# Performance work log

Hardware: AMD Instinct MI355X
Metric: run time of the kernel (lower is better)

Reference implementation:

```python
import jax, jax.numpy as jnp
import numpy as np

N_NODES = 100000
N_EDGES = 3200000
F_IN = 128
HIDDEN = 16
F_OUT = 2


def setup_inputs() -> dict:
    key = jax.random.key(0)
    k1, k2, k3, k4 = jax.random.split(key, 4)
    x = jax.random.normal(k1, (N_NODES, F_IN), dtype=jnp.float32)
    edge_index = jax.random.randint(k2, (2, N_EDGES), 0, N_NODES, dtype=jnp.int64)
    # Glorot-ish init like torch_geometric's GCNConv linear layers
    W1 = jax.random.normal(k3, (F_IN, HIDDEN), dtype=jnp.float32) * (1.0 / np.sqrt(F_IN))
    b1 = jnp.zeros((HIDDEN,), dtype=jnp.float32)
    W2 = jax.random.normal(k4, (HIDDEN, F_OUT), dtype=jnp.float32) * (1.0 / np.sqrt(HIDDEN))
    b2 = jnp.zeros((F_OUT,), dtype=jnp.float32)
    return {"x": x, "edge_index": edge_index, "W1": W1, "b1": b1, "W2": W2, "b2": b2}


def _gcn_conv(x, src, dst, W, b, num_nodes):
    """PyG GCNConv: out = D^{-1/2}(A+I)D^{-1/2} X W + b (self-loops included in src/dst)."""
    h = x @ W  # [N, F_out]
    ones = jnp.ones(src.shape[0], dtype=h.dtype)
    deg = jax.ops.segment_sum(ones, dst, num_segments=num_nodes)  # in-degree incl. self-loop
    deg_inv_sqrt = jnp.where(deg > 0, jax.lax.rsqrt(jnp.maximum(deg, 1.0)), 0.0)
    norm = deg_inv_sqrt[src] * deg_inv_sqrt[dst]  # [E+N]
    msg = h[src] * norm[:, None]  # gather + scale: [E+N, F_out]
    out = jax.ops.segment_sum(msg, dst, num_segments=num_nodes)  # scatter-add
    return out + b


def reference(x, edge_index, W1, b1, W2, b2):
    num_nodes = x.shape[0]
    self_loops = jnp.arange(num_nodes, dtype=edge_index.dtype)
    src = jnp.concatenate([edge_index[0], self_loops])
    dst = jnp.concatenate([edge_index[1], self_loops])
    h = jax.nn.relu(_gcn_conv(x, src, dst, W1, b1, num_nodes))
    # F.dropout(training=self.training) is identity in eval mode
    out = _gcn_conv(h, src, dst, W2, b2, num_nodes)
    return out
```

## Files before the change

### kernel.cpp

```cpp
#include <hip/hip_runtime.h>

#define N_NODES 100000
#define N_EDGES 3200000
#define F_IN    128
#define HIDDEN  16
#define F_OUT   2

#define BSZ     128
#define NB      782
#define NPAD    (NB * BSZ)
#define G       512
#define EPB     (N_EDGES / G)
#define DUMMY_E 100000u

typedef float  f32x4 __attribute__((ext_vector_type(4)));
typedef float  f32x2 __attribute__((ext_vector_type(2)));
typedef _Float16 half8 __attribute__((ext_vector_type(8)));
typedef _Float16 half4 __attribute__((ext_vector_type(4)));

__global__ __launch_bounds__(256) void k_hist(const int* __restrict__ dst,
                                              unsigned* __restrict__ blockHist) {
    __shared__ unsigned hist[NB];
    int t = threadIdx.x, g = blockIdx.x;
    for (int i = t; i < NB; i += 256) hist[i] = 0u;
    __syncthreads();
    int base = g * EPB;
    for (int i = t; i < EPB; i += 256) atomicAdd(&hist[dst[base + i] >> 7], 1u);
    __syncthreads();
    for (int i = t; i < NB; i += 256) blockHist[i * G + g] = hist[i];
}

__global__ __launch_bounds__(G) void k_scan_blocks(unsigned* __restrict__ blockHist,
                                                   unsigned* __restrict__ total) {
    __shared__ unsigned s[G];
    int b = blockIdx.x, t = threadIdx.x;
    unsigned v = blockHist[b * G + t];
    s[t] = v;
    __syncthreads();
    for (int off = 1; off < G; off <<= 1) {
        unsigned xv = (t >= off) ? s[t - off] : 0u;
        __syncthreads();
        s[t] += xv;
        __syncthreads();
    }
    blockHist[b * G + t] = s[t] - v;
    if (t == G - 1) total[b] = s[t];
}

__global__ __launch_bounds__(1024) void k_scan_buckets(const unsigned* __restrict__ total,
                                                       unsigned* __restrict__ bucketBase,
                                                       int* __restrict__ rowstart) {
    __shared__ unsigned s[1024];
    int t = threadIdx.x;
    unsigned v = (t < NB) ? total[t] : 0u;
    s[t] = v;
    __syncthreads();
    for (int off = 1; off < 1024; off <<= 1) {
        unsigned xv = (t >= off) ? s[t - off] : 0u;
        __syncthreads();
        s[t] += xv;
        __syncthreads();
    }
    if (t < NB) bucketBase[t] = s[t] - v;
    if (t == 1023) {
        bucketBase[NB] = s[t];
        rowstart[N_NODES] = (int)s[t];
    }
}

__global__ __launch_bounds__(256) void k_scatter(const int* __restrict__ src,
                                                 const int* __restrict__ dst,
                                                 const unsigned* __restrict__ blockHist,
                                                 const unsigned* __restrict__ bucketBase,
                                                 unsigned* __restrict__ adj) {
    __shared__ unsigned stage[EPB];
    __shared__ unsigned short stage_b[EPB];
    __shared__ unsigned hist[NB];
    __shared__ unsigned lstart[NB];
    __shared__ unsigned gbase[NB];
    __shared__ unsigned ssum[256];
    int t = threadIdx.x, g = blockIdx.x;
    for (int i = t; i < NB; i += 256) {
        hist[i] = 0u;
        gbase[i] = bucketBase[i] + blockHist[i * G + g];
    }
    __syncthreads();
    int base = g * EPB;
    const int* srcg = src + base;
    const int* dstg = dst + base;
    for (int i = t; i < EPB; i += 256) atomicAdd(&hist[(unsigned)dstg[i] >> 7], 1u);
    __syncthreads();
    int i0 = t * 4;
    unsigned v0 = (i0 + 0 < NB) ? hist[i0 + 0] : 0u;
    unsigned v1 = (i0 + 1 < NB) ? hist[i0 + 1] : 0u;
    unsigned v2 = (i0 + 2 < NB) ? hist[i0 + 2] : 0u;
    unsigned v3 = (i0 + 3 < NB) ? hist[i0 + 3] : 0u;
    unsigned my = v0 + v1 + v2 + v3;
    ssum[t] = my;
    __syncthreads();
    for (int off = 1; off < 256; off <<= 1) {
        unsigned xv = (t >= off) ? ssum[t - off] : 0u;
        __syncthreads();
        ssum[t] += xv;
        __syncthreads();
    }
    unsigned e0 = ssum[t] - my;
    __syncthreads();
    unsigned e1 = e0 + v0, e2 = e1 + v1, e3 = e2 + v2;
    if (i0 + 0 < NB) { lstart[i0 + 0] = e0; hist[i0 + 0] = e0; }
    if (i0 + 1 < NB) { lstart[i0 + 1] = e1; hist[i0 + 1] = e1; }
    if (i0 + 2 < NB) { lstart[i0 + 2] = e2; hist[i0 + 2] = e2; }
    if (i0 + 3 < NB) { lstart[i0 + 3] = e3; hist[i0 + 3] = e3; }
    __syncthreads();
    for (int i = t; i < EPB; i += 256) {
        int s = srcg[i], d = dstg[i];
        unsigned bkt = (unsigned)d >> 7;
        unsigned pos = atomicAdd(&hist[bkt], 1u);
        stage[pos] = ((unsigned)(d & 127) << 17) | (unsigned)s;
        stage_b[pos] = (unsigned short)bkt;
    }
    __syncthreads();
    for (int j = t; j < EPB; j += 256) {
        unsigned bkt = stage_b[j];
        adj[gbase[bkt] + (j - lstart[bkt])] = stage[j];
    }
}

__global__ __launch_bounds__(256) void k_sortbucket(const unsigned* __restrict__ adj,
                                                    const unsigned* __restrict__ bucketBase,
                                                    unsigned* __restrict__ adj2,
                                                    int* __restrict__ rowstart,
                                                    float* __restrict__ dinv) {
    __shared__ unsigned hist[BSZ];
    __shared__ unsigned sc[BSZ];
    __shared__ unsigned cur[BSZ];
    int b = blockIdx.x, t = threadIdx.x;
    if (t < BSZ) hist[t] = 0u;
    __syncthreads();
    int e0 = (int)bucketBase[b], e1 = (int)bucketBase[b + 1];
    for (int i = e0 + t; i < e1; i += 256) atomicAdd(&hist[adj[i] >> 17], 1u);
    __syncthreads();
    if (t < BSZ) sc[t] = hist[t];
    __syncthreads();
    for (int off = 1; off < BSZ; off <<= 1) {
        unsigned a = 0;
        if (t < BSZ && t >= off) a = sc[t - off];
        __syncthreads();
        if (t < BSZ) sc[t] += a;
        __syncthreads();
    }
    if (t < BSZ) {
        unsigned excl = sc[t] - hist[t];
        cur[t] = (unsigned)e0 + excl;
        int node = b * BSZ + t;
        if (node < N_NODES) {
            rowstart[node] = e0 + (int)excl;
            dinv[node] = rsqrtf((float)(hist[t] + 1u));
        }
    }
    __syncthreads();
    for (int i = e0 + t; i < e1; i += 256) {
        unsigned v = adj[i];
        unsigned pos = atomicAdd(&cur[v >> 17], 1u);
        adj2[pos] = v & 0x1FFFFu;
    }
}

#define MM1_NODES 64
#define SXP 132
__global__ __launch_bounds__(256) void k_mm1(const float* __restrict__ x,
                                             const float* __restrict__ W1,
                                             const float* __restrict__ dinv,
                                             half4* __restrict__ hs) {
    __shared__ float sW[F_IN * HIDDEN];
    __shared__ float sX[MM1_NODES * SXP];
    int t = threadIdx.x;
    for (int i = t; i < F_IN * HIDDEN; i += 256) sW[i] = W1[i];
    int node0 = blockIdx.x * MM1_NODES;
    const float4* xv = (const float4*)(x + (size_t)node0 * F_IN);
    int maxv = (N_NODES - node0) * (F_IN / 4);
    if (maxv < 0) maxv = 0;
    for (int i = t; i < MM1_NODES * (F_IN / 4); i += 256) {
        if (i < maxv) {
            int nl = i >> 5, f4 = i & 31;
            ((float4*)(sX + nl * SXP))[f4] = xv[i];
        }
    }
    __syncthreads();
    int lane4 = t & 3;
    int nl = t >> 2;
    int n = node0 + nl;
    if (n >= NPAD) return;
    if (n >= N_NODES) {
        half4 hz = {(_Float16)0.f, (_Float16)0.f, (_Float16)0.f, (_Float16)0.f};
        hs[(size_t)n * 4 + lane4] = hz;
        return;
    }
    const float4* sWv = (const float4*)sW;
    float4 a = {0.f, 0.f, 0.f, 0.f};
    #pragma unroll 8
    for (int f = 0; f < F_IN; ++f) {
        float xval = sX[nl * SXP + f];
        float4 w = sWv[f * 4 + lane4];
        a.x = fmaf(xval, w.x, a.x);
        a.y = fmaf(xval, w.y, a.y);
        a.z = fmaf(xval, w.z, a.z);
        a.w = fmaf(xval, w.w, a.w);
    }
    float dv = dinv[n];
    half4 h; h[0] = (_Float16)(a.x * dv); h[1] = (_Float16)(a.y * dv);
    h[2] = (_Float16)(a.z * dv); h[3] = (_Float16)(a.w * dv);
    hs[(size_t)n * 4 + lane4] = h;
}

__global__ __launch_bounds__(256) void k_agg1(const unsigned* __restrict__ adj2,
                                              const int* __restrict__ rowstart,
                                              const char* __restrict__ hs,
                                              const float* __restrict__ dinv,
                                              float* __restrict__ out1) {
    int g = blockIdx.x * 256 + threadIdx.x;
    int node = g >> 1, le = g & 1;
    if (node >= N_NODES) return;
    int rs = rowstart[node], re = rowstart[node + 1];
    unsigned le16 = (unsigned)le * 16u;
    unsigned dummy_off = DUMMY_E * 32u + le16;

    float a0 = 0.f, a1 = 0.f, a2 = 0.f, a3 = 0.f, a4 = 0.f, a5 = 0.f, a6 = 0.f, a7 = 0.f;
    f32x4 w0, w1, w2, w3, w4, w5, w6, w7;

#define GL1(dst, o) asm volatile("global_load_dwordx4 %0, %1, %2" \
    : "=v"(dst) : "v"(o), "s"(hs) : "memory");
#define AC1(w_) { half8 h8; __builtin_memcpy(&h8, &w_, 16); \
    a0 += (float)h8[0]; a1 += (float)h8[1]; a2 += (float)h8[2]; a3 += (float)h8[3]; \
    a4 += (float)h8[4]; a5 += (float)h8[5]; a6 += (float)h8[6]; a7 += (float)h8[7]; }

    for (int bs = rs; bs < re; bs += 8) {
        const unsigned* ap = adj2 + bs;
        unsigned j0 = ap[0], j1 = ap[1], j2 = ap[2], j3 = ap[3];
        unsigned j4 = ap[4], j5 = ap[5], j6 = ap[6], j7 = ap[7];
        unsigned o0 = (bs + 0 < re) ? (j0 << 5) + le16 : dummy_off;
        unsigned o1 = (bs + 1 < re) ? (j1 << 5) + le16 : dummy_off;
        unsigned o2 = (bs + 2 < re) ? (j2 << 5) + le16 : dummy_off;
        unsigned o3 = (bs + 3 < re) ? (j3 << 5) + le16 : dummy_off;
        unsigned o4 = (bs + 4 < re) ? (j4 << 5) + le16 : dummy_off;
        unsigned o5 = (bs + 5 < re) ? (j5 << 5) + le16 : dummy_off;
        unsigned o6 = (bs + 6 < re) ? (j6 << 5) + le16 : dummy_off;
        unsigned o7 = (bs + 7 < re) ? (j7 << 5) + le16 : dummy_off;
        GL1(w0, o0) GL1(w1, o1) GL1(w2, o2) GL1(w3, o3)
        GL1(w4, o4) GL1(w5, o5) GL1(w6, o6) GL1(w7, o7)
        asm volatile("s_waitcnt vmcnt(0)" ::: "memory");
        __builtin_amdgcn_sched_barrier(0);
        AC1(w0) AC1(w1) AC1(w2) AC1(w3) AC1(w4) AC1(w5) AC1(w6) AC1(w7)
    }
    const _Float16* selfrow = (const _Float16*)(hs + (size_t)node * 32 + le16);
    float dv = dinv[node];
    float4 q0, q1;
    q0.x = dv * (a0 + (float)selfrow[0]); q0.y = dv * (a1 + (float)selfrow[1]);
    q0.z = dv * (a2 + (float)selfrow[2]); q0.w = dv * (a3 + (float)selfrow[3]);
    q1.x = dv * (a4 + (float)selfrow[4]); q1.y = dv * (a5 + (float)selfrow[5]);
    q1.z = dv * (a6 + (float)selfrow[6]); q1.w = dv * (a7 + (float)selfrow[7]);
    float* op = out1 + (size_t)node * HIDDEN + le * 8;
    *(float4*)(op + 0) = q0;
    *(float4*)(op + 4) = q1;
}

__global__ __launch_bounds__(256) void k_mm2(const float* __restrict__ out1,
                                             const float* __restrict__ b1,
                                             const float* __restrict__ W2,
                                             const float* __restrict__ dinv,
                                             float2* __restrict__ hs2) {
    int n = blockIdx.x * 256 + threadIdx.x;
    if (n >= NPAD) return;
    if (n >= N_NODES) {
        float2 z = {0.f, 0.f};
        hs2[n] = z;
        return;
    }
    float a0 = 0.f, a1 = 0.f;
    #pragma unroll
    for (int kk = 0; kk < HIDDEN; ++kk) {
        float v = fmaxf(out1[(size_t)n * HIDDEN + kk] + b1[kk], 0.f);
        a0 = fmaf(v, W2[kk * F_OUT + 0], a0);
        a1 = fmaf(v, W2[kk * F_OUT + 1], a1);
    }
    float dv = dinv[n];
    float2 h2; h2.x = a0 * dv; h2.y = a1 * dv;
    hs2[n] = h2;
}

__global__ __launch_bounds__(256) void k_agg2(const unsigned* __restrict__ adj2,
                                              const int* __restrict__ rowstart,
                                              const char* __restrict__ hs2,
                                              const float* __restrict__ dinv,
                                              const float* __restrict__ b2,
                                              float2* __restrict__ out) {
    int node = blockIdx.x * 256 + threadIdx.x;
    if (node >= N_NODES) return;
    int rs = rowstart[node], re = rowstart[node + 1];
    unsigned dummy_off = DUMMY_E * 8u;

    float a0 = 0.f, a1 = 0.f;
    f32x2 w0, w1, w2, w3, w4, w5, w6, w7;

#define GL2(dst, o) asm volatile("global_load_dwordx2 %0, %1, %2" \
    : "=v"(dst) : "v"(o), "s"(hs2) : "memory");

    for (int bs = rs; bs < re; bs += 8) {
        const unsigned* ap = adj2 + bs;
        unsigned j0 = ap[0], j1 = ap[1], j2 = ap[2], j3 = ap[3];
        unsigned j4 = ap[4], j5 = ap[5], j6 = ap[6], j7 = ap[7];
        unsigned o0 = (bs + 0 < re) ? (j0 << 3) : dummy_off;
        unsigned o1 = (bs + 1 < re) ? (j1 << 3) : dummy_off;
        unsigned o2 = (bs + 2 < re) ? (j2 << 3) : dummy_off;
        unsigned o3 = (bs + 3 < re) ? (j3 << 3) : dummy_off;
        unsigned o4 = (bs + 4 < re) ? (j4 << 3) : dummy_off;
        unsigned o5 = (bs + 5 < re) ? (j5 << 3) : dummy_off;
        unsigned o6 = (bs + 6 < re) ? (j6 << 3) : dummy_off;
        unsigned o7 = (bs + 7 < re) ? (j7 << 3) : dummy_off;
        GL2(w0, o0) GL2(w1, o1) GL2(w2, o2) GL2(w3, o3)
        GL2(w4, o4) GL2(w5, o5) GL2(w6, o6) GL2(w7, o7)
        asm volatile("s_waitcnt vmcnt(0)" ::: "memory");
        __builtin_amdgcn_sched_barrier(0);
        a0 += w0[0] + w1[0] + w2[0] + w3[0] + w4[0] + w5[0] + w6[0] + w7[0];
        a1 += w0[1] + w1[1] + w2[1] + w3[1] + w4[1] + w5[1] + w6[1] + w7[1];
    }
    const float2* h2p = (const float2*)hs2;
    float2 selfv = h2p[node];
    float dv = dinv[node];
    float2 r;
    r.x = fmaf(dv, a0 + selfv.x, b2[0]);
    r.y = fmaf(dv, a1 + selfv.y, b2[1]);
    out[node] = r;
}

extern "C" void kernel_launch(void* const* d_in, const int* in_sizes, int n_in,
                              void* d_out, int out_size, void* d_ws, size_t ws_size,
                              hipStream_t stream) {
    const float* x   = (const float*)d_in[0];
    const int*   ei  = (const int*)d_in[1];
    const int*   srcv = ei;
    const int*   dstv = ei + N_EDGES;
    const float* W1  = (const float*)d_in[2];
    const float* b1  = (const float*)d_in[3];
    const float* W2  = (const float*)d_in[4];
    const float* b2  = (const float*)d_in[5];
    float* out = (float*)d_out;

    char* w = (char*)d_ws;
    unsigned* adj        = (unsigned*)w;  w += (size_t)N_EDGES * 4;
    float*    out1       = (float*)adj;
    unsigned* adj2       = (unsigned*)w;  w += (size_t)(N_EDGES + 8) * 4;
    unsigned* blockHist  = (unsigned*)w;  w += (size_t)NB * G * 4;
    unsigned* total      = (unsigned*)w;  w += (size_t)NB * 4;
    unsigned* bucketBase = (unsigned*)w;  w += (size_t)(NB + 1) * 4;
    int*      rowstart   = (int*)w;       w += (size_t)(N_NODES + 1) * 4;
    w = (char*)(((size_t)w + 15) & ~(size_t)15);
    float* dinv  = (float*)w;  w += (size_t)N_NODES * 4;
    char*  hs    = w;          w += (size_t)NPAD * HIDDEN * 2;
    float* hs2   = (float*)w;

    k_hist        <<<G, 256, 0, stream>>>(dstv, blockHist);
    k_scan_blocks <<<NB, G, 0, stream>>>(blockHist, total);
    k_scan_buckets<<<1, 1024, 0, stream>>>(total, bucketBase, rowstart);
    k_scatter     <<<G, 256, 0, stream>>>(srcv, dstv, blockHist, bucketBase, adj);
    k_sortbucket  <<<NB, 256, 0, stream>>>(adj, bucketBase, adj2, rowstart, dinv);
    k_mm1         <<<NPAD / MM1_NODES, 256, 0, stream>>>(x, W1, dinv, (half4*)hs);
    k_agg1        <<<(2 * NPAD) / 256, 256, 0, stream>>>(adj2, rowstart, hs, dinv, out1);
    k_mm2         <<<(NPAD + 255) / 256, 256, 0, stream>>>(out1, b1, W2, dinv, (float2*)hs2);
    k_agg2        <<<(NPAD + 255) / 256, 256, 0, stream>>>(adj2, rowstart, (const char*)hs2,
                                                           dinv, b2, (float2*)out);
}
```

Measured before the change: 138.3 us.

## Fuse second-layer transform into agg1, widen buckets, and split shared histograms

Folds the bias, ReLU and W2 projection into the first aggregation kernel, using a lane-pair shuffle to reduce the two halves. This removes the k_mm2 launch and the round trip of the 16-wide intermediate through global memory. The bucket size doubles to 256 nodes, so the bucket count halves, and the scan kernels and sort blocks are resized to match. Histogram kernels now read int2 and alternate threads between two shared histograms to reduce atomic contention. The catch is that each bucket sort block has more work and uses larger shared buffers.

```diff
diff --git a/kernel.cpp b/kernel.cpp
--- a/kernel.cpp
+++ b/kernel.cpp
@@ -6,8 +6,8 @@
 #define HIDDEN  16
 #define F_OUT   2
 
-#define BSZ     128
-#define NB      782
+#define BSZ     256
+#define NB      391
 #define NPAD    (NB * BSZ)
 #define G       512
 #define EPB     (N_EDGES / G)
@@ -20,14 +20,20 @@
 
 __global__ __launch_bounds__(256) void k_hist(const int* __restrict__ dst,
                                               unsigned* __restrict__ blockHist) {
-    __shared__ unsigned hist[NB];
+    __shared__ unsigned h0[NB];
+    __shared__ unsigned h1[NB];
     int t = threadIdx.x, g = blockIdx.x;
-    for (int i = t; i < NB; i += 256) hist[i] = 0u;
-    __syncthreads();
-    int base = g * EPB;
-    for (int i = t; i < EPB; i += 256) atomicAdd(&hist[dst[base + i] >> 7], 1u);
-    __syncthreads();
-    for (int i = t; i < NB; i += 256) blockHist[i * G + g] = hist[i];
+    for (int i = t; i < NB; i += 256) { h0[i] = 0u; h1[i] = 0u; }
+    __syncthreads();
+    const int2* d2 = (const int2*)(dst + g * EPB);
+    unsigned* myh = (t & 1) ? h1 : h0;
+    for (int i = t; i < EPB / 2; i += 256) {
+        int2 v = d2[i];
+        atomicAdd(&myh[(unsigned)v.x >> 8], 1u);
+        atomicAdd(&myh[(unsigned)v.y >> 8], 1u);
+    }
+    __syncthreads();
+    for (int i = t; i < NB; i += 256) blockHist[i * G + g] = h0[i] + h1[i];
 }
 
 __global__ __launch_bounds__(G) void k_scan_blocks(unsigned* __restrict__ blockHist,
@@ -47,22 +53,22 @@
     if (t == G - 1) total[b] = s[t];
 }
 
-__global__ __launch_bounds__(1024) void k_scan_buckets(const unsigned* __restrict__ total,
-                                                       unsigned* __restrict__ bucketBase,
-                                                       int* __restrict__ rowstart) {
-    __shared__ unsigned s[1024];
+__global__ __launch_bounds__(512) void k_scan_buckets(const unsigned* __restrict__ total,
+                                                      unsigned* __restrict__ bucketBase,
+                                                      int* __restrict__ rowstart) {
+    __shared__ unsigned s[512];
     int t = threadIdx.x;
     unsigned v = (t < NB) ? total[t] : 0u;
     s[t] = v;
     __syncthreads();
-    for (int off = 1; off < 1024; off <<= 1) {
+    for (int off = 1; off < 512; off <<= 1) {
         unsigned xv = (t >= off) ? s[t - off] : 0u;
         __syncthreads();
         s[t] += xv;
         __syncthreads();
     }
     if (t < NB) bucketBase[t] = s[t] - v;
-    if (t == 1023) {
+    if (t == 511) {
         bucketBase[NB] = s[t];
         rowstart[N_NODES] = (int)s[t];
     }
@@ -76,26 +82,29 @@
     __shared__ unsigned stage[EPB];
     __shared__ unsigned short stage_b[EPB];
     __shared__ unsigned hist[NB];
+    __shared__ unsigned h1[NB];
     __shared__ unsigned lstart[NB];
     __shared__ unsigned gbase[NB];
     __shared__ unsigned ssum[256];
     int t = threadIdx.x, g = blockIdx.x;
     for (int i = t; i < NB; i += 256) {
-        hist[i] = 0u;
+        hist[i] = 0u; h1[i] = 0u;
         gbase[i] = bucketBase[i] + blockHist[i * G + g];
     }
     __syncthreads();
-    int base = g * EPB;
-    const int* srcg = src + base;
-    const int* dstg = dst + base;
-    for (int i = t; i < EPB; i += 256) atomicAdd(&hist[(unsigned)dstg[i] >> 7], 1u);
-    __syncthreads();
-    int i0 = t * 4;
-    unsigned v0 = (i0 + 0 < NB) ? hist[i0 + 0] : 0u;
-    unsigned v1 = (i0 + 1 < NB) ? hist[i0 + 1] : 0u;
-    unsigned v2 = (i0 + 2 < NB) ? hist[i0 + 2] : 0u;
-    unsigned v3 = (i0 + 3 < NB) ? hist[i0 + 3] : 0u;
-    unsigned my = v0 + v1 + v2 + v3;
+    const int2* s2 = (const int2*)(src + g * EPB);
+    const int2* d2 = (const int2*)(dst + g * EPB);
+    unsigned* myh = (t & 1) ? h1 : hist;
+    for (int i = t; i < EPB / 2; i += 256) {
+        int2 v = d2[i];
+        atomicAdd(&myh[(unsigned)v.x >> 8], 1u);
+        atomicAdd(&myh[(unsigned)v.y >> 8], 1u);
+    }
+    __syncthreads();
+    int i0 = t * 2;
+    unsigned v0 = (i0 + 0 < NB) ? hist[i0 + 0] + h1[i0 + 0] : 0u;
+    unsigned v1 = (i0 + 1 < NB) ? hist[i0 + 1] + h1[i0 + 1] : 0u;
+    unsigned my = v0 + v1;
     ssum[t] = my;
     __syncthreads();
     for (int off = 1; off < 256; off <<= 1) {
@@ -106,18 +115,20 @@
     }
     unsigned e0 = ssum[t] - my;
     __syncthreads();
-    unsigned e1 = e0 + v0, e2 = e1 + v1, e3 = e2 + v2;
+    unsigned e1 = e0 + v0;
     if (i0 + 0 < NB) { lstart[i0 + 0] = e0; hist[i0 + 0] = e0; }
     if (i0 + 1 < NB) { lstart[i0 + 1] = e1; hist[i0 + 1] = e1; }
-    if (i0 + 2 < NB) { lstart[i0 + 2] = e2; hist[i0 + 2] = e2; }
-    if (i0 + 3 < NB) { lstart[i0 + 3] = e3; hist[i0 + 3] = e3; }
-    __syncthreads();
-    for (int i = t; i < EPB; i += 256) {
-        int s = srcg[i], d = dstg[i];
-        unsigned bkt = (unsigned)d >> 7;
-        unsigned pos = atomicAdd(&hist[bkt], 1u);
-        stage[pos] = ((unsigned)(d & 127) << 17) | (unsigned)s;
-        stage_b[pos] = (unsigned short)bkt;
+    __syncthreads();
+    for (int i = t; i < EPB / 2; i += 256) {
+        int2 sv = s2[i], dv = d2[i];
+        unsigned bkt0 = (unsigned)dv.x >> 8;
+        unsigned pos0 = atomicAdd(&hist[bkt0], 1u);
+        stage[pos0] = ((unsigned)(dv.x & 255) << 17) | (unsigned)sv.x;
+        stage_b[pos0] = (unsigned short)bkt0;
+        unsigned bkt1 = (unsigned)dv.y >> 8;
+        unsigned pos1 = atomicAdd(&hist[bkt1], 1u);
+        stage[pos1] = ((unsigned)(dv.y & 255) << 17) | (unsigned)sv.y;
+        stage_b[pos1] = (unsigned short)bkt1;
     }
     __syncthreads();
     for (int j = t; j < EPB; j += 256) {
@@ -135,28 +146,25 @@
     __shared__ unsigned sc[BSZ];
     __shared__ unsigned cur[BSZ];
     int b = blockIdx.x, t = threadIdx.x;
-    if (t < BSZ) hist[t] = 0u;
+    hist[t] = 0u;
     __syncthreads();
     int e0 = (int)bucketBase[b], e1 = (int)bucketBase[b + 1];
     for (int i = e0 + t; i < e1; i += 256) atomicAdd(&hist[adj[i] >> 17], 1u);
     __syncthreads();
-    if (t < BSZ) sc[t] = hist[t];
+    sc[t] = hist[t];
     __syncthreads();
     for (int off = 1; off < BSZ; off <<= 1) {
-        unsigned a = 0;
-        if (t < BSZ && t >= off) a = sc[t - off];
-        __syncthreads();
-        if (t < BSZ) sc[t] += a;
-        __syncthreads();
-    }
-    if (t < BSZ) {
-        unsigned excl = sc[t] - hist[t];
-        cur[t] = (unsigned)e0 + excl;
-        int node = b * BSZ + t;
-        if (node < N_NODES) {
-            rowstart[node] = e0 + (int)excl;
-            dinv[node] = rsqrtf((float)(hist[t] + 1u));
-        }
+        unsigned a = (t >= off) ? sc[t - off] : 0u;
+        __syncthreads();
+        sc[t] += a;
+        __syncthreads();
+    }
+    unsigned excl = sc[t] - hist[t];
+    cur[t] = (unsigned)e0 + excl;
+    int node = b * BSZ + t;
+    if (node < N_NODES) {
+        rowstart[node] = e0 + (int)excl;
+        dinv[node] = rsqrtf((float)(hist[t] + 1u));
     }
     __syncthreads();
     for (int i = e0 + t; i < e1; i += 256) {
@@ -217,10 +225,15 @@
                                               const int* __restrict__ rowstart,
                                               const char* __restrict__ hs,
                                               const float* __restrict__ dinv,
-                                              float* __restrict__ out1) {
+                                              const float* __restrict__ b1,
+                                              const float* __restrict__ W2,
+                                              float2* __restrict__ hs2) {
     int g = blockIdx.x * 256 + threadIdx.x;
     int node = g >> 1, le = g & 1;
-    if (node >= N_NODES) return;
+    if (node >= N_NODES) {
+        if (le == 0 && node < NPAD) { float2 z = {0.f, 0.f}; hs2[node] = z; }
+        return;
+    }
     int rs = rowstart[node], re = rowstart[node + 1];
     unsigned le16 = (unsigned)le * 16u;
     unsigned dummy_off = DUMMY_E * 32u + le16;
@@ -254,38 +267,29 @@
     }
     const _Float16* selfrow = (const _Float16*)(hs + (size_t)node * 32 + le16);
     float dv = dinv[node];
-    float4 q0, q1;
-    q0.x = dv * (a0 + (float)selfrow[0]); q0.y = dv * (a1 + (float)selfrow[1]);
-    q0.z = dv * (a2 + (float)selfrow[2]); q0.w = dv * (a3 + (float)selfrow[3]);
-    q1.x = dv * (a4 + (float)selfrow[4]); q1.y = dv * (a5 + (float)selfrow[5]);
-    q1.z = dv * (a6 + (float)selfrow[6]); q1.w = dv * (a7 + (float)selfrow[7]);
-    float* op = out1 + (size_t)node * HIDDEN + le * 8;
-    *(float4*)(op + 0) = q0;
-    *(float4*)(op + 4) = q1;
-}
-
-__global__ __launch_bounds__(256) void k_mm2(const float* __restrict__ out1,
-                                             const float* __restrict__ b1,
-                                             const float* __restrict__ W2,
-                                             const float* __restrict__ dinv,
-                                             float2* __restrict__ hs2) {
-    int n = blockIdx.x * 256 + threadIdx.x;
-    if (n >= NPAD) return;
-    if (n >= N_NODES) {
-        float2 z = {0.f, 0.f};
-        hs2[n] = z;
-        return;
-    }
-    float a0 = 0.f, a1 = 0.f;
-    #pragma unroll
-    for (int kk = 0; kk < HIDDEN; ++kk) {
-        float v = fmaxf(out1[(size_t)n * HIDDEN + kk] + b1[kk], 0.f);
-        a0 = fmaf(v, W2[kk * F_OUT + 0], a0);
-        a1 = fmaf(v, W2[kk * F_OUT + 1], a1);
-    }
-    float dv = dinv[n];
-    float2 h2; h2.x = a0 * dv; h2.y = a1 * dv;
-    hs2[n] = h2;
+    float q0 = dv * (a0 + (float)selfrow[0]), q1 = dv * (a1 + (float)selfrow[1]);
+    float q2 = dv * (a2 + (float)selfrow[2]), q3 = dv * (a3 + (float)selfrow[3]);
+    float q4 = dv * (a4 + (float)selfrow[4]), q5 = dv * (a5 + (float)selfrow[5]);
+    float q6 = dv * (a6 + (float)selfrow[6]), q7 = dv * (a7 + (float)selfrow[7]);
+    const float4* b1v = (const float4*)(b1 + le * 8);
+    float4 ba = b1v[0], bb = b1v[1];
+    const float4* w2v = (const float4*)(W2 + le * 16);
+    float4 wA = w2v[0], wB = w2v[1], wC = w2v[2], wD = w2v[3];
+    float p0 = 0.f, p1 = 0.f, r;
+    r = fmaxf(q0 + ba.x, 0.f); p0 = fmaf(r, wA.x, p0); p1 = fmaf(r, wA.y, p1);
+    r = fmaxf(q1 + ba.y, 0.f); p0 = fmaf(r, wA.z, p0); p1 = fmaf(r, wA.w, p1);
+    r = fmaxf(q2 + ba.z, 0.f); p0 = fmaf(r, wB.x, p0); p1 = fmaf(r, wB.y, p1);
+    r = fmaxf(q3 + ba.w, 0.f); p0 = fmaf(r, wB.z, p0); p1 = fmaf(r, wB.w, p1);
+    r = fmaxf(q4 + bb.x, 0.f); p0 = fmaf(r, wC.x, p0); p1 = fmaf(r, wC.y, p1);
+    r = fmaxf(q5 + bb.y, 0.f); p0 = fmaf(r, wC.z, p0); p1 = fmaf(r, wC.w, p1);
+    r = fmaxf(q6 + bb.z, 0.f); p0 = fmaf(r, wD.x, p0); p1 = fmaf(r, wD.y, p1);
+    r = fmaxf(q7 + bb.w, 0.f); p0 = fmaf(r, wD.z, p0); p1 = fmaf(r, wD.w, p1);
+    p0 += __shfl_xor(p0, 1);
+    p1 += __shfl_xor(p1, 1);
+    if (le == 0) {
+        float2 h2; h2.x = p0 * dv; h2.y = p1 * dv;
+        hs2[node] = h2;
+    }
 }
 
 __global__ __launch_bounds__(256) void k_agg2(const unsigned* __restrict__ adj2,
@@ -348,7 +352,6 @@
 
     char* w = (char*)d_ws;
     unsigned* adj        = (unsigned*)w;  w += (size_t)N_EDGES * 4;
-    float*    out1       = (float*)adj;
     unsigned* adj2       = (unsigned*)w;  w += (size_t)(N_EDGES + 8) * 4;
     unsigned* blockHist  = (unsigned*)w;  w += (size_t)NB * G * 4;
     unsigned* total      = (unsigned*)w;  w += (size_t)NB * 4;
@@ -361,12 +364,12 @@
 
     k_hist        <<<G, 256, 0, stream>>>(dstv, blockHist);
     k_scan_blocks <<<NB, G, 0, stream>>>(blockHist, total);
-    k_scan_buckets<<<1, 1024, 0, stream>>>(total, bucketBase, rowstart);
+    k_scan_buckets<<<1, 512, 0, stream>>>(total, bucketBase, rowstart);
     k_scatter     <<<G, 256, 0, stream>>>(srcv, dstv, blockHist, bucketBase, adj);
     k_sortbucket  <<<NB, 256, 0, stream>>>(adj, bucketBase, adj2, rowstart, dinv);
     k_mm1         <<<NPAD / MM1_NODES, 256, 0, stream>>>(x, W1, dinv, (half4*)hs);
-    k_agg1        <<<(2 * NPAD) / 256, 256, 0, stream>>>(adj2, rowstart, hs, dinv, out1);
-    k_mm2         <<<(NPAD + 255) / 256, 256, 0, stream>>>(out1, b1, W2, dinv, (float2*)hs2);
+    k_agg1        <<<(2 * NPAD) / 256, 256, 0, stream>>>(adj2, rowstart, hs, dinv,
+                                                         b1, W2, (float2*)hs2);
     k_agg2        <<<(NPAD + 255) / 256, 256, 0, stream>>>(adj2, rowstart, (const char*)hs2,
                                                            dinv, b2, (float2*)out);
 }
```

After: 126.8 us. -8.3%, faster.
